# Kernel optimization log

Measured on AMD Instinct MI355X. Metric: run time of the kernel, lower is better.

Reference implementation:

```python
import jax, jax.numpy as jnp
import numpy as np

D = 512
B = 8
S1 = 2048
S2 = 2048


def _rope_cos_sin(seq_len, dim, dtype=jnp.float32):
    half = dim // 2
    inv_freq = 1.0 / (10000.0 ** (jnp.arange(half, dtype=jnp.float32) / half))
    t = jnp.arange(seq_len, dtype=jnp.float32)
    freqs = jnp.outer(t, inv_freq)                      # [S, D/2]
    emb = jnp.concatenate([freqs, freqs], axis=-1)      # [S, D]
    return jnp.cos(emb).astype(dtype), jnp.sin(emb).astype(dtype)


def _rotate_half(x):
    half = x.shape[-1] // 2
    return jnp.concatenate([-x[..., half:], x[..., :half]], axis=-1)


def _apply_rope(x, cos, sin):
    # x: [B, S, D]; cos/sin: [S, D]
    return x * cos[None, :, :] + _rotate_half(x) * sin[None, :, :]


def setup_inputs() -> dict:
    key = jax.random.key(0)
    ks = jax.random.split(key, 12)
    s = 1.0 / np.sqrt(D)
    return {
        "h1": jax.random.normal(ks[0], (B, S1, D), dtype=jnp.float32),
        "h2": jax.random.normal(ks[1], (B, S2, D), dtype=jnp.float32),
        "Wq": jax.random.normal(ks[2], (D, D), dtype=jnp.float32) * s,
        "bq": jnp.zeros((D,), dtype=jnp.float32),
        "Wk": jax.random.normal(ks[3], (D, D), dtype=jnp.float32) * s,
        "bk": jnp.zeros((D,), dtype=jnp.float32),
        "Wv": jax.random.normal(ks[4], (D, D), dtype=jnp.float32) * s,
        "bv": jnp.zeros((D,), dtype=jnp.float32),
        "Wo": jax.random.normal(ks[5], (D, D), dtype=jnp.float32) * s,
        "bo": jnp.zeros((D,), dtype=jnp.float32),
    }


def reference(h1, h2, Wq, bq, Wk, bk, Wv, bv, Wo, bo):
    d = h1.shape[-1]
    # Linear projections (torch Linear: x @ W.T + b)
    q = jnp.einsum("bsd,ed->bse", h1, Wq) + bq
    k = jnp.einsum("bsd,ed->bse", h2, Wk) + bk
    v = jnp.einsum("bsd,ed->bse", h2, Wv) + bv
    # RoPE on full hidden dim (single head)
    cos_q, sin_q = _rope_cos_sin(q.shape[1], d)
    cos_k, sin_k = _rope_cos_sin(k.shape[1], d)
    q = _apply_rope(q, cos_q, sin_q)
    k = _apply_rope(k, cos_k, sin_k)
    # scaled dot-product attention with full score matrix (faithful to source)
    energy = jnp.einsum("bqd,bkd->bqk", q, k) / jnp.sqrt(jnp.float32(d))
    attn = jax.nn.softmax(energy, axis=-1)
    out = jnp.einsum("bqk,bkd->bqd", attn, v)
    return jnp.einsum("bsd,ed->bse", out, Wo) + bo
```

## Files before the change

kernel.cpp:

```cpp
#include <hip/hip_runtime.h>
#include <stdint.h>

#define SCALE_E 0.044194173824159216f
#define LOG2_10000 13.287712379549449f
#define MCONST 8.0f

typedef __bf16 bf16x8 __attribute__((ext_vector_type(8)));
typedef float  f32x4  __attribute__((ext_vector_type(4)));

#define MFMA16(a, b, c) __builtin_amdgcn_mfma_f32_16x16x32_bf16((a), (b), (c), 0, 0, 0)

__device__ __forceinline__ void gload_lds16(const void* gp, void* lp) {
  __builtin_amdgcn_global_load_lds(
      reinterpret_cast<const uint32_t __attribute__((address_space(1)))*>(
          reinterpret_cast<uintptr_t>(gp)),
      reinterpret_cast<uint32_t __attribute__((address_space(3)))*>(
          reinterpret_cast<uintptr_t>(lp)),
      16, 0, 0);
}

__global__ __launch_bounds__(256) void gemm_split(
    const float* __restrict__ A, const float* __restrict__ W,
    const float* __restrict__ bias, float* __restrict__ C, int M)
{
  __shared__ __align__(16) __bf16 Als[2 * 512 * 8];
  __shared__ __align__(16) __bf16 Wls[2 * 512 * 8];

  const int t    = threadIdx.x;
  const int lane = t & 63;
  const int w    = t >> 6;
  const int m    = lane & 15;
  const int quad = lane >> 4;
  const int mw   = w & 1;
  const int nw   = w >> 1;
  const int m0   = blockIdx.y * 128;
  const int n0   = blockIdx.x * 128;

  const float* Ap0 = A + (size_t)(m0 + w * 16 + m) * 512 + quad * 8;
  const float* Ap1 = A + (size_t)(m0 + (w + 4) * 16 + m) * 512 + quad * 8;
  const float* Wp0 = W + (size_t)(n0 + w * 16 + m) * 512 + quad * 8;
  const float* Wp1 = W + (size_t)(n0 + (w + 4) * 16 + m) * 512 + quad * 8;

  f32x4 acc[4][4] = {};

  float4 ra[4], rw_[4];
  ra[0] = *(const float4*)(Ap0);     ra[1] = *(const float4*)(Ap0 + 4);
  ra[2] = *(const float4*)(Ap1);     ra[3] = *(const float4*)(Ap1 + 4);
  rw_[0] = *(const float4*)(Wp0);    rw_[1] = *(const float4*)(Wp0 + 4);
  rw_[2] = *(const float4*)(Wp1);    rw_[3] = *(const float4*)(Wp1 + 4);

  for (int kt = 0; kt < 512; kt += 32) {
    __syncthreads();
    #pragma unroll
    for (int h = 0; h < 2; ++h) {
      int slot = t + 256 * h;
      float v[8] = {ra[2*h].x, ra[2*h].y, ra[2*h].z, ra[2*h].w,
                    ra[2*h+1].x, ra[2*h+1].y, ra[2*h+1].z, ra[2*h+1].w};
      float u[8] = {rw_[2*h].x, rw_[2*h].y, rw_[2*h].z, rw_[2*h].w,
                    rw_[2*h+1].x, rw_[2*h+1].y, rw_[2*h+1].z, rw_[2*h+1].w};
      bf16x8 ah, al, bh, bl;
      #pragma unroll
      for (int j = 0; j < 8; ++j) {
        __bf16 hv = (__bf16)v[j];
        ah[j] = hv; al[j] = (__bf16)(v[j] - (float)hv);
        __bf16 hu = (__bf16)u[j];
        bh[j] = hu; bl[j] = (__bf16)(u[j] - (float)hu);
      }
      *(bf16x8*)&Als[(size_t)slot * 8]         = ah;
      *(bf16x8*)&Als[(size_t)(512 + slot) * 8] = al;
      *(bf16x8*)&Wls[(size_t)slot * 8]         = bh;
      *(bf16x8*)&Wls[(size_t)(512 + slot) * 8] = bl;
    }
    __syncthreads();

    if (kt + 32 < 512) {
      ra[0] = *(const float4*)(Ap0 + kt + 32);  ra[1] = *(const float4*)(Ap0 + kt + 36);
      ra[2] = *(const float4*)(Ap1 + kt + 32);  ra[3] = *(const float4*)(Ap1 + kt + 36);
      rw_[0] = *(const float4*)(Wp0 + kt + 32); rw_[1] = *(const float4*)(Wp0 + kt + 36);
      rw_[2] = *(const float4*)(Wp1 + kt + 32); rw_[3] = *(const float4*)(Wp1 + kt + 36);
    }

    bf16x8 ah[4], al[4], bh[4], bl[4];
    #pragma unroll
    for (int mt = 0; mt < 4; ++mt) {
      ah[mt] = *(const bf16x8*)&Als[(size_t)((mw * 4 + mt) * 64 + lane) * 8];
      al[mt] = *(const bf16x8*)&Als[(size_t)(512 + (mw * 4 + mt) * 64 + lane) * 8];
    }
    #pragma unroll
    for (int nt = 0; nt < 4; ++nt) {
      bh[nt] = *(const bf16x8*)&Wls[(size_t)((nw * 4 + nt) * 64 + lane) * 8];
      bl[nt] = *(const bf16x8*)&Wls[(size_t)(512 + (nw * 4 + nt) * 64 + lane) * 8];
    }
    #pragma unroll
    for (int mt = 0; mt < 4; ++mt)
      #pragma unroll
      for (int nt = 0; nt < 4; ++nt) {
        acc[mt][nt] = MFMA16(al[mt], bh[nt], acc[mt][nt]);
        acc[mt][nt] = MFMA16(ah[mt], bl[nt], acc[mt][nt]);
        acc[mt][nt] = MFMA16(ah[mt], bh[nt], acc[mt][nt]);
      }
  }

  float bv[4];
  #pragma unroll
  for (int nt = 0; nt < 4; ++nt) bv[nt] = bias[n0 + (nw * 4 + nt) * 16 + m];

  #pragma unroll
  for (int mt = 0; mt < 4; ++mt)
    #pragma unroll
    for (int r = 0; r < 4; ++r) {
      size_t row = m0 + (mw * 4 + mt) * 16 + quad * 4 + r;
      float* cp = C + row * 512 + n0;
      #pragma unroll
      for (int nt = 0; nt < 4; ++nt)
        cp[(nw * 4 + nt) * 16 + m] = acc[mt][nt][r] + bv[nt];
    }
}

__global__ __launch_bounds__(256) void rope_cast(
    const float* __restrict__ X, __bf16* __restrict__ Y, float scale)
{
  const int row = blockIdx.x;
  const int s = row & 2047;
  const int j = threadIdx.x;
  const float* p = X + (size_t)row * 512;
  __bf16* q = Y + (size_t)row * 512;
  float invf = exp2f((float)j * (-LOG2_10000 / 256.0f));
  float ang = (float)s * invf;
  float c = cosf(ang), sn = sinf(ang);
  float x1 = p[j], x2 = p[j + 256];
  q[j]       = (__bf16)((x1 * c - x2 * sn) * scale);
  q[j + 256] = (__bf16)((x2 * c + x1 * sn) * scale);
}

__global__ __launch_bounds__(256) void cast_transpose_v(
    const float* __restrict__ V, __bf16* __restrict__ Vt)
{
  __shared__ float tile[32][33];
  const int b  = blockIdx.z;
  const int s0 = blockIdx.x * 32;
  const int d0 = blockIdx.y * 32;
  const float* Vb = V + (size_t)b * 2048 * 512;
  __bf16* Vtb = Vt + (size_t)b * 512 * 2048;

  #pragma unroll
  for (int r = 0; r < 4; ++r) {
    int s = s0 + threadIdx.y + 8 * r;
    tile[threadIdx.y + 8 * r][threadIdx.x] = Vb[(size_t)s * 512 + d0 + threadIdx.x];
  }
  __syncthreads();
  #pragma unroll
  for (int r = 0; r < 4; ++r) {
    int d = d0 + threadIdx.y + 8 * r;
    Vtb[(size_t)d * 2048 + s0 + threadIdx.x] = (__bf16)tile[threadIdx.x][threadIdx.y + 8 * r];
  }
}

__global__ __launch_bounds__(512, 2) void attn_mfma(
    const __bf16* __restrict__ Qb, const __bf16* __restrict__ Kb,
    const __bf16* __restrict__ Vt, float* __restrict__ O)
{
  __shared__ __align__(16) __bf16 Kbuf[4096 * 8];
  __shared__ __align__(16) __bf16 Ps[4096];
  __shared__ float l_sh[128];

  const int t    = threadIdx.x;
  const int b    = blockIdx.x & 7;
  const int q0   = (blockIdx.x >> 3) * 64;
  const int w    = t >> 6;
  const int lane = t & 63;
  const int m    = lane & 15;
  const int quad = lane >> 4;
  const int rw   = w >> 1;
  const int kp   = w & 1;

  const __bf16* Kbase = Kb + (size_t)b * 2048 * 512;
  const __bf16* Vbase = Vt + (size_t)b * 512 * 2048;

  const __bf16* qrow = Qb + ((size_t)b * 2048 + q0 + rw * 16 + m) * 512 + quad * 8;
  bf16x8 qf[16];
  #pragma unroll
  for (int kb = 0; kb < 16; ++kb) qf[kb] = *(const bf16x8*)(qrow + kb * 32);

  bf16x8 onesf;
  #pragma unroll
  for (int j = 0; j < 8; ++j) onesf[j] = (__bf16)1.0f;

  f32x4 o_acc[4][4] = {};
  f32x4 l_tile = {0.f, 0.f, 0.f, 0.f};

  const __bf16* vrow = Vbase + (size_t)(w * 64 + m) * 2048;

  const __bf16* lsrc = &Ps[(size_t)((rw * 2 + kp) * 64 + lane) * 8];

  #pragma unroll
  for (int i = 0; i < 8; ++i) {
    const int j = w * 8 + i;
    gload_lds16(Kbase + (size_t)((j & 3) * 16 + m) * 512 + (j >> 2) * 32 + quad * 8,
                &Kbuf[(size_t)(j * 64 + lane) * 8]);
  }

  for (int kt = 0; kt < 2048; kt += 64) {
    __syncthreads();

    bf16x8 vf[8];
    #pragma unroll
    for (int dt = 0; dt < 4; ++dt)
      #pragma unroll
      for (int kh = 0; kh < 2; ++kh)
        vf[dt * 2 + kh] =
            *(const bf16x8*)(vrow + (size_t)dt * 16 * 2048 + kt + kh * 32 + quad * 8);

    f32x4 sc0 = {0.f, 0.f, 0.f, 0.f}, sc1 = {0.f, 0.f, 0.f, 0.f};
    __builtin_amdgcn_s_setprio(1);
    #pragma unroll
    for (int kb = 0; kb < 16; ++kb) {
      bf16x8 k0 = *(const bf16x8*)&Kbuf[(size_t)((kb * 4 + kp * 2 + 0) * 64 + lane) * 8];
      bf16x8 k1 = *(const bf16x8*)&Kbuf[(size_t)((kb * 4 + kp * 2 + 1) * 64 + lane) * 8];
      sc0 = MFMA16(qf[kb], k0, sc0);
      sc1 = MFMA16(qf[kb], k1, sc1);
    }
    __builtin_amdgcn_s_setprio(0);

    #pragma unroll
    for (int g = 0; g < 2; ++g) {
      const int kg = kp * 2 + g;
      f32x4 sc = g ? sc1 : sc0;
      float p0 = __expf(sc[0] - MCONST);
      float p1 = __expf(sc[1] - MCONST);
      float p2 = __expf(sc[2] - MCONST);
      float p3 = __expf(sc[3] - MCONST);
      __bf16* pw = &Ps[(size_t)(((rw * 2 + (kg >> 1)) * 4 + ((kg & 1) * 2 + (m >> 3))) * 16
                                + quad * 4) * 8 + (m & 7)];
      pw[0]  = (__bf16)p0;
      pw[8]  = (__bf16)p1;
      pw[16] = (__bf16)p2;
      pw[24] = (__bf16)p3;
    }

    __syncthreads();

    if (kt + 64 < 2048) {
      #pragma unroll
      for (int i = 0; i < 8; ++i) {
        const int j = w * 8 + i;
        gload_lds16(Kbase + (size_t)(kt + 64 + (j & 3) * 16 + m) * 512 + (j >> 2) * 32 + quad * 8,
                    &Kbuf[(size_t)(j * 64 + lane) * 8]);
      }
    }

    __builtin_amdgcn_s_setprio(1);

    {
      bf16x8 lf = *(const bf16x8*)lsrc;
      l_tile = MFMA16(lf, onesf, l_tile);
    }

    #pragma unroll
    for (int kh = 0; kh < 2; ++kh) {
      bf16x8 pf0 = *(const bf16x8*)&Ps[(size_t)((0 * 2 + kh) * 64 + lane) * 8];
      bf16x8 pf1 = *(const bf16x8*)&Ps[(size_t)((1 * 2 + kh) * 64 + lane) * 8];
      bf16x8 pf2 = *(const bf16x8*)&Ps[(size_t)((2 * 2 + kh) * 64 + lane) * 8];
      bf16x8 pf3 = *(const bf16x8*)&Ps[(size_t)((3 * 2 + kh) * 64 + lane) * 8];
      #pragma unroll
      for (int dt = 0; dt < 4; ++dt) {
        bf16x8 vv = vf[dt * 2 + kh];
        o_acc[0][dt] = MFMA16(pf0, vv, o_acc[0][dt]);
        o_acc[1][dt] = MFMA16(pf1, vv, o_acc[1][dt]);
        o_acc[2][dt] = MFMA16(pf2, vv, o_acc[2][dt]);
        o_acc[3][dt] = MFMA16(pf3, vv, o_acc[3][dt]);
      }
    }
    __builtin_amdgcn_s_setprio(0);
  }

  if (m == 0) {
    #pragma unroll
    for (int r = 0; r < 4; ++r)
      l_sh[kp * 64 + rw * 16 + quad * 4 + r] = l_tile[r];
  }
  __syncthreads();
  #pragma unroll
  for (int rt = 0; rt < 4; ++rt) {
    float invl[4];
    #pragma unroll
    for (int r = 0; r < 4; ++r)
      invl[r] = 1.0f / (l_sh[rt * 16 + quad * 4 + r] + l_sh[64 + rt * 16 + quad * 4 + r]);
    #pragma unroll
    for (int dt = 0; dt < 4; ++dt)
      #pragma unroll
      for (int r = 0; r < 4; ++r) {
        size_t row = (size_t)b * 2048 + q0 + rt * 16 + quad * 4 + r;
        O[row * 512 + w * 64 + dt * 16 + m] = o_acc[rt][dt][r] * invl[r];
      }
  }
}

extern "C" void kernel_launch(void* const* d_in, const int* in_sizes, int n_in,
                              void* d_out, int out_size, void* d_ws, size_t ws_size,
                              hipStream_t stream)
{
  const float* h1 = (const float*)d_in[0];
  const float* h2 = (const float*)d_in[1];
  const float* Wq = (const float*)d_in[2];
  const float* bq = (const float*)d_in[3];
  const float* Wk = (const float*)d_in[4];
  const float* bk = (const float*)d_in[5];
  const float* Wv = (const float*)d_in[6];
  const float* bv = (const float*)d_in[7];
  const float* Wo = (const float*)d_in[8];
  const float* bo = (const float*)d_in[9];
  float* out = (float*)d_out;

  const size_t MB = 1024 * 1024;

  float*  Qf  = (float*)d_ws;
  float*  Kf  = (float*)((char*)d_ws + 32 * MB);
  float*  O2  = (float*)((char*)d_ws + 16 * MB);
  __bf16* Vtb = (__bf16*)d_ws;
  __bf16* Qbb = (__bf16*)((char*)d_ws + 64 * MB);
  __bf16* Kbb = (__bf16*)((char*)d_ws + 80 * MB);
  float*  Vf  = out;

  const int M = 8 * 2048;
  dim3 gG(4, M / 128);

  gemm_split<<<gG, 256, 0, stream>>>(h1, Wq, bq, Qf, M);
  gemm_split<<<gG, 256, 0, stream>>>(h2, Wk, bk, Kf, M);
  gemm_split<<<gG, 256, 0, stream>>>(h2, Wv, bv, Vf, M);
  rope_cast<<<M, 256, 0, stream>>>(Qf, Qbb, SCALE_E);
  rope_cast<<<M, 256, 0, stream>>>(Kf, Kbb, 1.0f);
  cast_transpose_v<<<dim3(64, 16, 8), dim3(32, 8), 0, stream>>>(Vf, Vtb);
  attn_mfma<<<256, 512, 0, stream>>>(Qbb, Kbb, Vtb, O2);
  gemm_split<<<gG, 256, 0, stream>>>(O2, Wo, bo, out, M);
}
```

Baseline: 418.1 us.

## Pre-split operands to bf16 hi/lo, fuse RoPE into GEMM epilogue, async LDS staging

Activations and weights are now pre-split into bf16 high/low pairs by separate kernels, so the GEMM streams bf16 data through double-buffered direct global-to-LDS loads instead of converting fp32 in registers each tile. Wq/Wk rows are permuted so rotate-half pairs land in adjacent lanes, which lets RoPE be applied in the GEMM epilogue via a lane shuffle and a precomputed cos/sin table. This removes the fp32 Q/K intermediates and the separate rope kernels. V is written directly as bf16 and attention emits a hi/lo output, in exchange for extra split passes and more workspace traffic.

```diff
diff --git a/kernel.cpp b/kernel.cpp
--- a/kernel.cpp
+++ b/kernel.cpp
@@ -19,12 +19,71 @@
       16, 0, 0);
 }
 
-__global__ __launch_bounds__(256) void gemm_split(
-    const float* __restrict__ A, const float* __restrict__ W,
-    const float* __restrict__ bias, float* __restrict__ C, int M)
-{
-  __shared__ __align__(16) __bf16 Als[2 * 512 * 8];
-  __shared__ __align__(16) __bf16 Wls[2 * 512 * 8];
+__global__ __launch_bounds__(256) void prep_w(
+    const float* __restrict__ Wq, const float* __restrict__ bq,
+    const float* __restrict__ Wk, const float* __restrict__ bk,
+    const float* __restrict__ Wv, const float* __restrict__ Wo,
+    __bf16* __restrict__ Wqph, __bf16* __restrict__ Wqpl,
+    __bf16* __restrict__ Wkph, __bf16* __restrict__ Wkpl,
+    __bf16* __restrict__ Wvh,  __bf16* __restrict__ Wvl,
+    __bf16* __restrict__ Woh,  __bf16* __restrict__ Wol,
+    float* __restrict__ bqp, float* __restrict__ bkp,
+    float2* __restrict__ tab)
+{
+  const int bid = blockIdx.x, t = threadIdx.x;
+  if (bid < 2048) {
+    const int widx = bid >> 9, e = bid & 511;
+    const float* src; __bf16 *dh, *dl; int srow = e;
+    if (widx == 0)      { src = Wq; dh = Wqph; dl = Wqpl; srow = (e >> 1) + (e & 1) * 256; }
+    else if (widx == 1) { src = Wk; dh = Wkph; dl = Wkpl; srow = (e >> 1) + (e & 1) * 256; }
+    else if (widx == 2) { src = Wv; dh = Wvh;  dl = Wvl; }
+    else                { src = Wo; dh = Woh;  dl = Wol; }
+    float2 v = ((const float2*)(src + (size_t)srow * 512))[t];
+    __bf16 h0 = (__bf16)v.x, h1 = (__bf16)v.y;
+    __bf16 l0 = (__bf16)(v.x - (float)h0), l1 = (__bf16)(v.y - (float)h1);
+    dh[(size_t)e * 512 + 2 * t]     = h0;
+    dh[(size_t)e * 512 + 2 * t + 1] = h1;
+    dl[(size_t)e * 512 + 2 * t]     = l0;
+    dl[(size_t)e * 512 + 2 * t + 1] = l1;
+    if (t == 0) {
+      if (widx == 0) bqp[e] = bq[srow];
+      if (widx == 1) bkp[e] = bk[srow];
+    }
+  } else {
+    const int s = bid - 2048;
+    const int i = t;
+    float invf = exp2f((float)i * (-LOG2_10000 / 256.0f));
+    float ang  = (float)s * invf;
+    tab[(size_t)s * 256 + i] = make_float2(cosf(ang), sinf(ang));
+  }
+}
+
+__global__ __launch_bounds__(256) void split_f32(
+    const float* __restrict__ X, __bf16* __restrict__ Xh, __bf16* __restrict__ Xl)
+{
+  const size_t i = ((size_t)blockIdx.x * 256 + threadIdx.x) * 8;
+  float4 a = *(const float4*)(X + i);
+  float4 b = *(const float4*)(X + i + 4);
+  float v[8] = {a.x, a.y, a.z, a.w, b.x, b.y, b.z, b.w};
+  bf16x8 h, l;
+  #pragma unroll
+  for (int j = 0; j < 8; ++j) {
+    __bf16 hv = (__bf16)v[j];
+    h[j] = hv;
+    l[j] = (__bf16)(v[j] - (float)hv);
+  }
+  *(bf16x8*)(Xh + i) = h;
+  *(bf16x8*)(Xl + i) = l;
+}
+
+template <int EPI>
+__global__ __launch_bounds__(256, 2) void gemm_ds(
+    const __bf16* __restrict__ Ah, const __bf16* __restrict__ Al,
+    const __bf16* __restrict__ Wh, const __bf16* __restrict__ Wl,
+    const float* __restrict__ bias, void* __restrict__ outp,
+    const float2* __restrict__ tab, float scale)
+{
+  __shared__ __align__(16) __bf16 LS[2][4][512 * 8];
 
   const int t    = threadIdx.x;
   const int lane = t & 63;
@@ -36,60 +95,45 @@
   const int m0   = blockIdx.y * 128;
   const int n0   = blockIdx.x * 128;
 
-  const float* Ap0 = A + (size_t)(m0 + w * 16 + m) * 512 + quad * 8;
-  const float* Ap1 = A + (size_t)(m0 + (w + 4) * 16 + m) * 512 + quad * 8;
-  const float* Wp0 = W + (size_t)(n0 + w * 16 + m) * 512 + quad * 8;
-  const float* Wp1 = W + (size_t)(n0 + (w + 4) * 16 + m) * 512 + quad * 8;
+  const __bf16* Ah0 = Ah + (size_t)(m0 + w * 16 + m) * 512 + quad * 8;
+  const __bf16* Ah1 = Ah + (size_t)(m0 + (w + 4) * 16 + m) * 512 + quad * 8;
+  const __bf16* Al0 = Al + (size_t)(m0 + w * 16 + m) * 512 + quad * 8;
+  const __bf16* Al1 = Al + (size_t)(m0 + (w + 4) * 16 + m) * 512 + quad * 8;
+  const __bf16* Wh0 = Wh + (size_t)(n0 + w * 16 + m) * 512 + quad * 8;
+  const __bf16* Wh1 = Wh + (size_t)(n0 + (w + 4) * 16 + m) * 512 + quad * 8;
+  const __bf16* Wl0 = Wl + (size_t)(n0 + w * 16 + m) * 512 + quad * 8;
+  const __bf16* Wl1 = Wl + (size_t)(n0 + (w + 4) * 16 + m) * 512 + quad * 8;
+
+  #define STAGE(bufi, kt) {                                                 \
+    gload_lds16(Ah0 + (kt), &LS[bufi][0][(size_t)t * 8]);                   \
+    gload_lds16(Ah1 + (kt), &LS[bufi][0][(size_t)(t + 256) * 8]);           \
+    gload_lds16(Al0 + (kt), &LS[bufi][1][(size_t)t * 8]);                   \
+    gload_lds16(Al1 + (kt), &LS[bufi][1][(size_t)(t + 256) * 8]);           \
+    gload_lds16(Wh0 + (kt), &LS[bufi][2][(size_t)t * 8]);                   \
+    gload_lds16(Wh1 + (kt), &LS[bufi][2][(size_t)(t + 256) * 8]);           \
+    gload_lds16(Wl0 + (kt), &LS[bufi][3][(size_t)t * 8]);                   \
+    gload_lds16(Wl1 + (kt), &LS[bufi][3][(size_t)(t + 256) * 8]);           \
+  }
 
   f32x4 acc[4][4] = {};
 
-  float4 ra[4], rw_[4];
-  ra[0] = *(const float4*)(Ap0);     ra[1] = *(const float4*)(Ap0 + 4);
-  ra[2] = *(const float4*)(Ap1);     ra[3] = *(const float4*)(Ap1 + 4);
-  rw_[0] = *(const float4*)(Wp0);    rw_[1] = *(const float4*)(Wp0 + 4);
-  rw_[2] = *(const float4*)(Wp1);    rw_[3] = *(const float4*)(Wp1 + 4);
-
-  for (int kt = 0; kt < 512; kt += 32) {
-    __syncthreads();
-    #pragma unroll
-    for (int h = 0; h < 2; ++h) {
-      int slot = t + 256 * h;
-      float v[8] = {ra[2*h].x, ra[2*h].y, ra[2*h].z, ra[2*h].w,
-                    ra[2*h+1].x, ra[2*h+1].y, ra[2*h+1].z, ra[2*h+1].w};
-      float u[8] = {rw_[2*h].x, rw_[2*h].y, rw_[2*h].z, rw_[2*h].w,
-                    rw_[2*h+1].x, rw_[2*h+1].y, rw_[2*h+1].z, rw_[2*h+1].w};
-      bf16x8 ah, al, bh, bl;
-      #pragma unroll
-      for (int j = 0; j < 8; ++j) {
-        __bf16 hv = (__bf16)v[j];
-        ah[j] = hv; al[j] = (__bf16)(v[j] - (float)hv);
-        __bf16 hu = (__bf16)u[j];
-        bh[j] = hu; bl[j] = (__bf16)(u[j] - (float)hu);
-      }
-      *(bf16x8*)&Als[(size_t)slot * 8]         = ah;
-      *(bf16x8*)&Als[(size_t)(512 + slot) * 8] = al;
-      *(bf16x8*)&Wls[(size_t)slot * 8]         = bh;
-      *(bf16x8*)&Wls[(size_t)(512 + slot) * 8] = bl;
-    }
-    __syncthreads();
-
-    if (kt + 32 < 512) {
-      ra[0] = *(const float4*)(Ap0 + kt + 32);  ra[1] = *(const float4*)(Ap0 + kt + 36);
-      ra[2] = *(const float4*)(Ap1 + kt + 32);  ra[3] = *(const float4*)(Ap1 + kt + 36);
-      rw_[0] = *(const float4*)(Wp0 + kt + 32); rw_[1] = *(const float4*)(Wp0 + kt + 36);
-      rw_[2] = *(const float4*)(Wp1 + kt + 32); rw_[3] = *(const float4*)(Wp1 + kt + 36);
-    }
+  STAGE(0, 0);
+  __syncthreads();
+
+  int cur = 0;
+  for (int ks = 0; ks < 16; ++ks) {
+    if (ks < 15) STAGE(cur ^ 1, (ks + 1) * 32);
 
     bf16x8 ah[4], al[4], bh[4], bl[4];
     #pragma unroll
     for (int mt = 0; mt < 4; ++mt) {
-      ah[mt] = *(const bf16x8*)&Als[(size_t)((mw * 4 + mt) * 64 + lane) * 8];
-      al[mt] = *(const bf16x8*)&Als[(size_t)(512 + (mw * 4 + mt) * 64 + lane) * 8];
+      ah[mt] = *(const bf16x8*)&LS[cur][0][(size_t)((mw * 4 + mt) * 64 + lane) * 8];
+      al[mt] = *(const bf16x8*)&LS[cur][1][(size_t)((mw * 4 + mt) * 64 + lane) * 8];
     }
     #pragma unroll
     for (int nt = 0; nt < 4; ++nt) {
-      bh[nt] = *(const bf16x8*)&Wls[(size_t)((nw * 4 + nt) * 64 + lane) * 8];
-      bl[nt] = *(const bf16x8*)&Wls[(size_t)(512 + (nw * 4 + nt) * 64 + lane) * 8];
+      bh[nt] = *(const bf16x8*)&LS[cur][2][(size_t)((nw * 4 + nt) * 64 + lane) * 8];
+      bl[nt] = *(const bf16x8*)&LS[cur][3][(size_t)((nw * 4 + nt) * 64 + lane) * 8];
     }
     #pragma unroll
     for (int mt = 0; mt < 4; ++mt)
@@ -99,48 +143,75 @@
         acc[mt][nt] = MFMA16(ah[mt], bl[nt], acc[mt][nt]);
         acc[mt][nt] = MFMA16(ah[mt], bh[nt], acc[mt][nt]);
       }
-  }
+
+    __syncthreads();
+    cur ^= 1;
+  }
+  #undef STAGE
 
   float bv[4];
   #pragma unroll
   for (int nt = 0; nt < 4; ++nt) bv[nt] = bias[n0 + (nw * 4 + nt) * 16 + m];
 
-  #pragma unroll
-  for (int mt = 0; mt < 4; ++mt)
-    #pragma unroll
-    for (int r = 0; r < 4; ++r) {
-      size_t row = m0 + (mw * 4 + mt) * 16 + quad * 4 + r;
-      float* cp = C + row * 512 + n0;
-      #pragma unroll
-      for (int nt = 0; nt < 4; ++nt)
-        cp[(nw * 4 + nt) * 16 + m] = acc[mt][nt][r] + bv[nt];
-    }
-}
-
-__global__ __launch_bounds__(256) void rope_cast(
-    const float* __restrict__ X, __bf16* __restrict__ Y, float scale)
-{
-  const int row = blockIdx.x;
-  const int s = row & 2047;
-  const int j = threadIdx.x;
-  const float* p = X + (size_t)row * 512;
-  __bf16* q = Y + (size_t)row * 512;
-  float invf = exp2f((float)j * (-LOG2_10000 / 256.0f));
-  float ang = (float)s * invf;
-  float c = cosf(ang), sn = sinf(ang);
-  float x1 = p[j], x2 = p[j + 256];
-  q[j]       = (__bf16)((x1 * c - x2 * sn) * scale);
-  q[j + 256] = (__bf16)((x2 * c + x1 * sn) * scale);
-}
-
-__global__ __launch_bounds__(256) void cast_transpose_v(
-    const float* __restrict__ V, __bf16* __restrict__ Vt)
-{
-  __shared__ float tile[32][33];
+  if constexpr (EPI == 0) {
+    float* C = (float*)outp;
+    #pragma unroll
+    for (int mt = 0; mt < 4; ++mt)
+      #pragma unroll
+      for (int r = 0; r < 4; ++r) {
+        size_t row = m0 + (mw * 4 + mt) * 16 + quad * 4 + r;
+        float* cp = C + row * 512 + n0;
+        #pragma unroll
+        for (int nt = 0; nt < 4; ++nt)
+          cp[(nw * 4 + nt) * 16 + m] = acc[mt][nt][r] + bv[nt];
+      }
+  } else if constexpr (EPI == 2) {
+    __bf16* C = (__bf16*)outp;
+    #pragma unroll
+    for (int mt = 0; mt < 4; ++mt)
+      #pragma unroll
+      for (int r = 0; r < 4; ++r) {
+        size_t row = m0 + (mw * 4 + mt) * 16 + quad * 4 + r;
+        __bf16* cp = C + row * 512 + n0;
+        #pragma unroll
+        for (int nt = 0; nt < 4; ++nt)
+          cp[(nw * 4 + nt) * 16 + m] = (__bf16)(acc[mt][nt][r] + bv[nt]);
+      }
+  } else {
+    __bf16* Y = (__bf16*)outp;
+    int ip[4];
+    #pragma unroll
+    for (int nt = 0; nt < 4; ++nt) ip[nt] = (n0 + (nw * 4 + nt) * 16 + m) >> 1;
+    const int half = m & 1;
+    #pragma unroll
+    for (int mt = 0; mt < 4; ++mt)
+      #pragma unroll
+      for (int r = 0; r < 4; ++r) {
+        int row  = m0 + (mw * 4 + mt) * 16 + quad * 4 + r;
+        int srow = row & 2047;
+        const float2* trow = tab + ((size_t)srow << 8);
+        __bf16* yp = Y + (size_t)row * 512 + n0;
+        #pragma unroll
+        for (int nt = 0; nt < 4; ++nt) {
+          float v  = acc[mt][nt][r] + bv[nt];
+          float px = __shfl_xor(v, 1);
+          float2 cs = trow[ip[nt]];
+          float o = half ? (v * cs.x + px * cs.y)
+                         : (v * cs.x - px * cs.y);
+          yp[(nw * 4 + nt) * 16 + m] = (__bf16)(o * scale);
+        }
+      }
+  }
+}
+
+__global__ __launch_bounds__(256) void transpose_v(
+    const __bf16* __restrict__ V, __bf16* __restrict__ Vt)
+{
+  __shared__ __bf16 tile[32][34];
   const int b  = blockIdx.z;
   const int s0 = blockIdx.x * 32;
   const int d0 = blockIdx.y * 32;
-  const float* Vb = V + (size_t)b * 2048 * 512;
+  const __bf16* Vb = V + (size_t)b * 2048 * 512;
   __bf16* Vtb = Vt + (size_t)b * 512 * 2048;
 
   #pragma unroll
@@ -152,13 +223,14 @@
   #pragma unroll
   for (int r = 0; r < 4; ++r) {
     int d = d0 + threadIdx.y + 8 * r;
-    Vtb[(size_t)d * 2048 + s0 + threadIdx.x] = (__bf16)tile[threadIdx.x][threadIdx.y + 8 * r];
+    Vtb[(size_t)d * 2048 + s0 + threadIdx.x] = tile[threadIdx.x][threadIdx.y + 8 * r];
   }
 }
 
 __global__ __launch_bounds__(512, 2) void attn_mfma(
     const __bf16* __restrict__ Qb, const __bf16* __restrict__ Kb,
-    const __bf16* __restrict__ Vt, float* __restrict__ O)
+    const __bf16* __restrict__ Vt, __bf16* __restrict__ Oh,
+    __bf16* __restrict__ Ol)
 {
   __shared__ __align__(16) __bf16 Kbuf[4096 * 8];
   __shared__ __align__(16) __bf16 Ps[4096];
@@ -190,7 +262,6 @@
   f32x4 l_tile = {0.f, 0.f, 0.f, 0.f};
 
   const __bf16* vrow = Vbase + (size_t)(w * 64 + m) * 2048;
-
   const __bf16* lsrc = &Ps[(size_t)((rw * 2 + kp) * 64 + lane) * 8];
 
   #pragma unroll
@@ -250,7 +321,6 @@
     }
 
     __builtin_amdgcn_s_setprio(1);
-
     {
       bf16x8 lf = *(const bf16x8*)lsrc;
       l_tile = MFMA16(lf, onesf, l_tile);
@@ -291,7 +361,11 @@
       #pragma unroll
       for (int r = 0; r < 4; ++r) {
         size_t row = (size_t)b * 2048 + q0 + rt * 16 + quad * 4 + r;
-        O[row * 512 + w * 64 + dt * 16 + m] = o_acc[rt][dt][r] * invl[r];
+        size_t idx = row * 512 + w * 64 + dt * 16 + m;
+        float o = o_acc[rt][dt][r] * invl[r];
+        __bf16 hi = (__bf16)o;
+        Oh[idx] = hi;
+        Ol[idx] = (__bf16)(o - (float)hi);
       }
   }
 }
@@ -313,24 +387,41 @@
   float* out = (float*)d_out;
 
   const size_t MB = 1024 * 1024;
-
-  float*  Qf  = (float*)d_ws;
-  float*  Kf  = (float*)((char*)d_ws + 32 * MB);
-  float*  O2  = (float*)((char*)d_ws + 16 * MB);
-  __bf16* Vtb = (__bf16*)d_ws;
-  __bf16* Qbb = (__bf16*)((char*)d_ws + 64 * MB);
-  __bf16* Kbb = (__bf16*)((char*)d_ws + 80 * MB);
-  float*  Vf  = out;
-
-  const int M = 8 * 2048;
-  dim3 gG(4, M / 128);
-
-  gemm_split<<<gG, 256, 0, stream>>>(h1, Wq, bq, Qf, M);
-  gemm_split<<<gG, 256, 0, stream>>>(h2, Wk, bk, Kf, M);
-  gemm_split<<<gG, 256, 0, stream>>>(h2, Wv, bv, Vf, M);
-  rope_cast<<<M, 256, 0, stream>>>(Qf, Qbb, SCALE_E);
-  rope_cast<<<M, 256, 0, stream>>>(Kf, Kbb, 1.0f);
-  cast_transpose_v<<<dim3(64, 16, 8), dim3(32, 8), 0, stream>>>(Vf, Vtb);
-  attn_mfma<<<256, 512, 0, stream>>>(Qbb, Kbb, Vtb, O2);
-  gemm_split<<<gG, 256, 0, stream>>>(O2, Wo, bo, out, M);
-}
+  char* ws = (char*)d_ws;
+
+  __bf16* Wqph = (__bf16*)(ws);
+  __bf16* Wqpl = (__bf16*)(ws + 512 * 1024);
+  __bf16* Wkph = (__bf16*)(ws + 1024 * 1024);
+  __bf16* Wkpl = (__bf16*)(ws + 1536 * 1024);
+  __bf16* Wvh  = (__bf16*)(ws + 2048 * 1024);
+  __bf16* Wvl  = (__bf16*)(ws + 2560 * 1024);
+  __bf16* Woh  = (__bf16*)(ws + 3072 * 1024);
+  __bf16* Wol  = (__bf16*)(ws + 3584 * 1024);
+  float2* tab  = (float2*)(ws + 4 * MB);
+  float*  bqp  = (float*)(ws + 8 * MB);
+  float*  bkp  = (float*)(ws + 8 * MB + 4096);
+  __bf16* h1h  = (__bf16*)(ws + 16 * MB);
+  __bf16* h1l  = (__bf16*)(ws + 32 * MB);
+  __bf16* h2h  = (__bf16*)(ws + 48 * MB);
+  __bf16* h2l  = (__bf16*)(ws + 64 * MB);
+  __bf16* Qbb  = (__bf16*)(ws + 80 * MB);
+  __bf16* Kbb  = (__bf16*)(ws + 16 * MB);
+  __bf16* Vbf  = (__bf16*)(ws + 32 * MB);
+  __bf16* Vtb  = (__bf16*)(ws + 48 * MB);
+  __bf16* O2h  = (__bf16*)(ws + 64 * MB);
+  __bf16* O2l  = (__bf16*)(ws + 32 * MB);
+
+  dim3 gG(4, 128);
+
+  prep_w<<<4096, 256, 0, stream>>>(Wq, bq, Wk, bk, Wv, Wo,
+                                   Wqph, Wqpl, Wkph, Wkpl, Wvh, Wvl, Woh, Wol,
+                                   bqp, bkp, tab);
+  split_f32<<<4096, 256, 0, stream>>>(h1, h1h, h1l);
+  split_f32<<<4096, 256, 0, stream>>>(h2, h2h, h2l);
+  gemm_ds<1><<<gG, 256, 0, stream>>>(h1h, h1l, Wqph, Wqpl, bqp, Qbb, tab, SCALE_E);
+  gemm_ds<1><<<gG, 256, 0, stream>>>(h2h, h2l, Wkph, Wkpl, bkp, Kbb, tab, 1.0f);
+  gemm_ds<2><<<gG, 256, 0, stream>>>(h2h, h2l, Wvh, Wvl, bv, Vbf, nullptr, 1.0f);
+  transpose_v<<<dim3(64, 16, 8), dim3(32, 8), 0, stream>>>(Vbf, Vtb);
+  attn_mfma<<<256, 512, 0, stream>>>(Qbb, Kbb, Vtb, O2h, O2l);
+  gemm_ds<0><<<gG, 256, 0, stream>>>(O2h, O2l, Woh, Wol, bo, out, nullptr, 1.0f);
+}
```

Result: slower. 436.3 us (+4.4%).

## Fuse RoPE and bf16 cast into QKV GEMM epilogue with permuted weights

Applied to the files above, without the earlier changes.

Permutes the Wq/Wk rows so each RoPE pair lands in adjacent columns, precomputes a cos/sin table, and applies RoPE plus the bf16 cast directly in the projection GEMM epilogue using lane shuffles. The three QKV projections become one launch (grid z=3), and V is written as bf16, so the transpose kernel now reads bf16. This removes the fp32 Q/K/V round trips through memory and several launches. In exchange it adds a small prep kernel that permutes the weights and builds the table on every call.

```diff
diff --git a/kernel.cpp b/kernel.cpp
--- a/kernel.cpp
+++ b/kernel.cpp
@@ -19,13 +19,40 @@
       16, 0, 0);
 }
 
-__global__ __launch_bounds__(256) void gemm_split(
+__global__ __launch_bounds__(256) void rope_prep(
+    const float* __restrict__ Wq, const float* __restrict__ bq,
+    const float* __restrict__ Wk, const float* __restrict__ bk,
+    float* __restrict__ Wqp, float* __restrict__ bqp,
+    float* __restrict__ Wkp, float* __restrict__ bkp,
+    float2* __restrict__ tab)
+{
+  const int bid = blockIdx.x, t = threadIdx.x;
+  if (bid < 1024) {
+    const float* W  = (bid < 512) ? Wq  : Wk;
+    const float* bb = (bid < 512) ? bq  : bk;
+    float* Wp       = (bid < 512) ? Wqp : Wkp;
+    float* bp       = (bid < 512) ? bqp : bkp;
+    const int e    = bid & 511;
+    const int orig = (e >> 1) + (e & 1) * 256;
+    const float2* s = (const float2*)(W + (size_t)orig * 512);
+    float2* d       = (float2*)(Wp + (size_t)e * 512);
+    d[t] = s[t];
+    if (t == 0) bp[e] = bb[orig];
+  } else {
+    const int s = bid - 1024;
+    const int i = t;
+    float invf = exp2f((float)i * (-LOG2_10000 / 256.0f));
+    float ang  = (float)s * invf;
+    tab[(size_t)s * 256 + i] = make_float2(cosf(ang), sinf(ang));
+  }
+}
+
+__device__ __forceinline__ void gemm_body(
     const float* __restrict__ A, const float* __restrict__ W,
-    const float* __restrict__ bias, float* __restrict__ C, int M)
-{
-  __shared__ __align__(16) __bf16 Als[2 * 512 * 8];
-  __shared__ __align__(16) __bf16 Wls[2 * 512 * 8];
-
+    const float* __restrict__ bias, int epi, void* __restrict__ outp,
+    const float2* __restrict__ tab, float scale,
+    __bf16* Als, __bf16* Wls)
+{
   const int t    = threadIdx.x;
   const int lane = t & 63;
   const int w    = t >> 6;
@@ -105,42 +132,94 @@
   #pragma unroll
   for (int nt = 0; nt < 4; ++nt) bv[nt] = bias[n0 + (nw * 4 + nt) * 16 + m];
 
-  #pragma unroll
-  for (int mt = 0; mt < 4; ++mt)
-    #pragma unroll
-    for (int r = 0; r < 4; ++r) {
-      size_t row = m0 + (mw * 4 + mt) * 16 + quad * 4 + r;
-      float* cp = C + row * 512 + n0;
-      #pragma unroll
-      for (int nt = 0; nt < 4; ++nt)
-        cp[(nw * 4 + nt) * 16 + m] = acc[mt][nt][r] + bv[nt];
-    }
-}
-
-__global__ __launch_bounds__(256) void rope_cast(
-    const float* __restrict__ X, __bf16* __restrict__ Y, float scale)
-{
-  const int row = blockIdx.x;
-  const int s = row & 2047;
-  const int j = threadIdx.x;
-  const float* p = X + (size_t)row * 512;
-  __bf16* q = Y + (size_t)row * 512;
-  float invf = exp2f((float)j * (-LOG2_10000 / 256.0f));
-  float ang = (float)s * invf;
-  float c = cosf(ang), sn = sinf(ang);
-  float x1 = p[j], x2 = p[j + 256];
-  q[j]       = (__bf16)((x1 * c - x2 * sn) * scale);
-  q[j + 256] = (__bf16)((x2 * c + x1 * sn) * scale);
-}
-
-__global__ __launch_bounds__(256) void cast_transpose_v(
-    const float* __restrict__ V, __bf16* __restrict__ Vt)
-{
-  __shared__ float tile[32][33];
+  if (epi == 0) {
+    float* C = (float*)outp;
+    #pragma unroll
+    for (int mt = 0; mt < 4; ++mt)
+      #pragma unroll
+      for (int r = 0; r < 4; ++r) {
+        size_t row = m0 + (mw * 4 + mt) * 16 + quad * 4 + r;
+        float* cp = C + row * 512 + n0;
+        #pragma unroll
+        for (int nt = 0; nt < 4; ++nt)
+          cp[(nw * 4 + nt) * 16 + m] = acc[mt][nt][r] + bv[nt];
+      }
+  } else if (epi == 2) {
+    __bf16* C = (__bf16*)outp;
+    #pragma unroll
+    for (int mt = 0; mt < 4; ++mt)
+      #pragma unroll
+      for (int r = 0; r < 4; ++r) {
+        size_t row = m0 + (mw * 4 + mt) * 16 + quad * 4 + r;
+        __bf16* cp = C + row * 512 + n0;
+        #pragma unroll
+        for (int nt = 0; nt < 4; ++nt)
+          cp[(nw * 4 + nt) * 16 + m] = (__bf16)(acc[mt][nt][r] + bv[nt]);
+      }
+  } else {
+    __bf16* Y = (__bf16*)outp;
+    int ip[4];
+    #pragma unroll
+    for (int nt = 0; nt < 4; ++nt) ip[nt] = (n0 + (nw * 4 + nt) * 16 + m) >> 1;
+    const int half = m & 1;
+    #pragma unroll
+    for (int mt = 0; mt < 4; ++mt)
+      #pragma unroll
+      for (int r = 0; r < 4; ++r) {
+        int row  = m0 + (mw * 4 + mt) * 16 + quad * 4 + r;
+        int srow = row & 2047;
+        const float2* trow = tab + ((size_t)srow << 8);
+        __bf16* yp = Y + (size_t)row * 512 + n0;
+        #pragma unroll
+        for (int nt = 0; nt < 4; ++nt) {
+          float v  = acc[mt][nt][r] + bv[nt];
+          float px = __shfl_xor(v, 1);
+          float2 cs = trow[ip[nt]];
+          float o = half ? (v * cs.x + px * cs.y)
+                         : (v * cs.x - px * cs.y);
+          yp[(nw * 4 + nt) * 16 + m] = (__bf16)(o * scale);
+        }
+      }
+  }
+}
+
+__global__ __launch_bounds__(256) void qkv_fused(
+    const float* __restrict__ h1, const float* __restrict__ h2,
+    const float* __restrict__ Wqp, const float* __restrict__ bqp,
+    const float* __restrict__ Wkp, const float* __restrict__ bkp,
+    const float* __restrict__ Wv,  const float* __restrict__ bv,
+    __bf16* __restrict__ Qbb, __bf16* __restrict__ Kbb,
+    __bf16* __restrict__ Vbf, const float2* __restrict__ tab)
+{
+  __shared__ __align__(16) __bf16 Als[2 * 512 * 8];
+  __shared__ __align__(16) __bf16 Wls[2 * 512 * 8];
+
+  const int z = blockIdx.z;
+  if (z == 0)
+    gemm_body(h1, Wqp, bqp, 1, Qbb, tab, SCALE_E, Als, Wls);
+  else if (z == 1)
+    gemm_body(h2, Wkp, bkp, 1, Kbb, tab, 1.0f, Als, Wls);
+  else
+    gemm_body(h2, Wv, bv, 2, Vbf, tab, 1.0f, Als, Wls);
+}
+
+__global__ __launch_bounds__(256) void gemm_o(
+    const float* __restrict__ A, const float* __restrict__ W,
+    const float* __restrict__ bias, float* __restrict__ C)
+{
+  __shared__ __align__(16) __bf16 Als[2 * 512 * 8];
+  __shared__ __align__(16) __bf16 Wls[2 * 512 * 8];
+  gemm_body(A, W, bias, 0, C, nullptr, 1.0f, Als, Wls);
+}
+
+__global__ __launch_bounds__(256) void transpose_v(
+    const __bf16* __restrict__ V, __bf16* __restrict__ Vt)
+{
+  __shared__ __bf16 tile[32][34];
   const int b  = blockIdx.z;
   const int s0 = blockIdx.x * 32;
   const int d0 = blockIdx.y * 32;
-  const float* Vb = V + (size_t)b * 2048 * 512;
+  const __bf16* Vb = V + (size_t)b * 2048 * 512;
   __bf16* Vtb = Vt + (size_t)b * 512 * 2048;
 
   #pragma unroll
@@ -152,7 +231,7 @@
   #pragma unroll
   for (int r = 0; r < 4; ++r) {
     int d = d0 + threadIdx.y + 8 * r;
-    Vtb[(size_t)d * 2048 + s0 + threadIdx.x] = (__bf16)tile[threadIdx.x][threadIdx.y + 8 * r];
+    Vtb[(size_t)d * 2048 + s0 + threadIdx.x] = tile[threadIdx.x][threadIdx.y + 8 * r];
   }
 }
 
@@ -190,7 +269,6 @@
   f32x4 l_tile = {0.f, 0.f, 0.f, 0.f};
 
   const __bf16* vrow = Vbase + (size_t)(w * 64 + m) * 2048;
-
   const __bf16* lsrc = &Ps[(size_t)((rw * 2 + kp) * 64 + lane) * 8];
 
   #pragma unroll
@@ -250,7 +328,6 @@
     }
 
     __builtin_amdgcn_s_setprio(1);
-
     {
       bf16x8 lf = *(const bf16x8*)lsrc;
       l_tile = MFMA16(lf, onesf, l_tile);
@@ -313,24 +390,23 @@
   float* out = (float*)d_out;
 
   const size_t MB = 1024 * 1024;
-
-  float*  Qf  = (float*)d_ws;
-  float*  Kf  = (float*)((char*)d_ws + 32 * MB);
-  float*  O2  = (float*)((char*)d_ws + 16 * MB);
-  __bf16* Vtb = (__bf16*)d_ws;
-  __bf16* Qbb = (__bf16*)((char*)d_ws + 64 * MB);
-  __bf16* Kbb = (__bf16*)((char*)d_ws + 80 * MB);
-  float*  Vf  = out;
-
-  const int M = 8 * 2048;
-  dim3 gG(4, M / 128);
-
-  gemm_split<<<gG, 256, 0, stream>>>(h1, Wq, bq, Qf, M);
-  gemm_split<<<gG, 256, 0, stream>>>(h2, Wk, bk, Kf, M);
-  gemm_split<<<gG, 256, 0, stream>>>(h2, Wv, bv, Vf, M);
-  rope_cast<<<M, 256, 0, stream>>>(Qf, Qbb, SCALE_E);
-  rope_cast<<<M, 256, 0, stream>>>(Kf, Kbb, 1.0f);
-  cast_transpose_v<<<dim3(64, 16, 8), dim3(32, 8), 0, stream>>>(Vf, Vtb);
+  char* ws = (char*)d_ws;
+
+  __bf16* Vbf = (__bf16*)(ws);
+  float*  Wqp = (float*)(ws + 16 * MB);
+  float*  Wkp = (float*)(ws + 17 * MB);
+  float*  bqp = (float*)(ws + 18 * MB);
+  float*  bkp = (float*)(ws + 18 * MB + 4096);
+  float2* tab = (float2*)(ws + 20 * MB);
+  __bf16* Vtb = (__bf16*)(ws + 32 * MB);
+  __bf16* Qbb = (__bf16*)(ws + 48 * MB);
+  __bf16* Kbb = (__bf16*)(ws + 64 * MB);
+  float*  O2  = (float*)(ws);
+
+  rope_prep<<<3072, 256, 0, stream>>>(Wq, bq, Wk, bk, Wqp, bqp, Wkp, bkp, tab);
+  qkv_fused<<<dim3(4, 128, 3), 256, 0, stream>>>(h1, h2, Wqp, bqp, Wkp, bkp,
+                                                 Wv, bv, Qbb, Kbb, Vbf, tab);
+  transpose_v<<<dim3(64, 16, 8), dim3(32, 8), 0, stream>>>(Vbf, Vtb);
   attn_mfma<<<256, 512, 0, stream>>>(Qbb, Kbb, Vtb, O2);
-  gemm_split<<<gG, 256, 0, stream>>>(O2, Wo, bo, out, M);
-}
+  gemm_o<<<dim3(4, 128), 256, 0, stream>>>(O2, Wo, bo, out);
+}
```

Measured after the change: 394.9 us. 5.6% less time.
